# Performance work log

Hardware: AMD Instinct MI355X
Metric: run time of the kernel (lower is better)

Reference implementation:

```python
import jax, jax.numpy as jnp
import numpy as np

IN_F, D_FC, D_H = 5, 32, 64

def setup_inputs() -> dict:
    key = jax.random.key(0)
    ks = jax.random.split(key, 10)
    B, T = 4096, 512
    s_fc = 1.0 / np.sqrt(IN_F)
    s_rnn = 1.0 / np.sqrt(D_H)
    s_out = 1.0 / np.sqrt(D_H)
    return {
        "x":    jax.random.normal(ks[0], (B, T, IN_F), dtype=jnp.float32),
        "W0":   jax.random.uniform(ks[1], (D_FC, IN_F), jnp.float32, -s_fc, s_fc),
        "b0":   jax.random.uniform(ks[2], (D_FC,), jnp.float32, -s_fc, s_fc),
        "W_ih": jax.random.uniform(ks[3], (4 * D_H, D_FC), jnp.float32, -s_rnn, s_rnn),
        "W_hh": jax.random.uniform(ks[4], (4 * D_H, D_H), jnp.float32, -s_rnn, s_rnn),
        "b_ih": jax.random.uniform(ks[5], (4 * D_H,), jnp.float32, -s_rnn, s_rnn),
        "b_hh": jax.random.uniform(ks[6], (4 * D_H,), jnp.float32, -s_rnn, s_rnn),
        "Wo":   jax.random.uniform(ks[7], (1, D_H), jnp.float32, -s_out, s_out),
        "bo":   jax.random.uniform(ks[8], (1,), jnp.float32, -s_out, s_out),
    }

def reference(x, W0, b0, W_ih, W_hh, b_ih, b_hh, Wo, bo):
    B, T, _ = x.shape
    # fc0: [B,T,5] -> [B,T,32]
    h0 = x @ W0.T + b0
    # Precompute input-side gate projections for all timesteps: [B,T,4H]
    xg = h0 @ W_ih.T + (b_ih + b_hh)
    xg_t = jnp.swapaxes(xg, 0, 1)  # [T,B,4H] for scan

    def step(carry, xg_step):
        h, c = carry
        gates = xg_step + h @ W_hh.T          # [B,4H]
        i, f, g, o = jnp.split(gates, 4, axis=-1)  # PyTorch gate order i,f,g,o
        i = jax.nn.sigmoid(i)
        f = jax.nn.sigmoid(f)
        g = jnp.tanh(g)
        o = jax.nn.sigmoid(o)
        c = f * c + i * g
        h = o * jnp.tanh(c)
        return (h, c), None

    init = (jnp.zeros((B, D_H), x.dtype), jnp.zeros((B, D_H), x.dtype))
    (h_last, _), _ = jax.lax.scan(step, init, xg_t)
    # out Linear on last timestep hidden: r_out[:, -1, :] == h_last
    return h_last @ Wo.T + bo  # [B,1]
```

## Files before the change

kernel.cpp:

```cpp
#include <hip/hip_runtime.h>

#define B_TOT   4096
#define T_STEPS 512
#define IN_F    5
#define D_FC    32
#define D_H     64
#define MB      16
#define NROW    16
#define ROWE    72

typedef _Float16 h8 __attribute__((ext_vector_type(8)));
typedef __fp16   h2 __attribute__((ext_vector_type(2)));
typedef float    f4 __attribute__((ext_vector_type(4)));

__device__ __forceinline__ float fexp2(float x) { return __builtin_amdgcn_exp2f(x); }
__device__ __forceinline__ float frcp(float x)  { return __builtin_amdgcn_rcpf(x); }

__device__ __forceinline__ void lstm_cell(
    float vi, float vf, float vg, float vo,
    float nbi, float nbf, float pbg, float nbo,
    float K1, float K2,
    float& cs, _Float16* dst)
{
    const float Ei = fexp2(fmaf(-K1, vi, nbi));
    const float Eg = fexp2(fmaf( K2, vg, pbg));
    const float Eo = fexp2(fmaf(-K1, vo, nbo));
    const float fg = frcp(1.0f + fexp2(fmaf(-K1, vf, nbf)));
    const float igg = (Eg - 1.0f) * frcp((1.0f + Ei) * (1.0f + Eg));
    cs = fmaf(fg, cs, igg);
    const float Ec = fexp2(K2 * cs);
    const float h  = (Ec - 1.0f) * frcp((1.0f + Eo) * (1.0f + Ec));
    *dst = (_Float16)h;
}

__global__ __launch_bounds__(256) void lstm_mfma(
    const float* __restrict__ x,
    const float* __restrict__ W0,
    const float* __restrict__ b0,
    const float* __restrict__ W_ih,
    const float* __restrict__ W_hh,
    const float* __restrict__ b_ih,
    const float* __restrict__ b_hh,
    const float* __restrict__ Wo,
    const float* __restrict__ bo,
    float* __restrict__ out)
{
    __shared__ __align__(16) _Float16 H[2][NROW][ROWE];

    const int tid  = threadIdx.x;
    const int lane = tid & 63;
    const int w    = tid >> 6;
    const int col  = lane & 15;
    const int quad = lane >> 4;
    const int bblk = blockIdx.x * MB;

    const float K1 = 1.4426950408889634f;
    const float K2 = 2.8853900817779268f;

    h8 Bf[4][2];
    #pragma unroll
    for (int q = 0; q < 4; ++q) {
        const int row = q * 64 + w * 16 + col;
        #pragma unroll
        for (int c = 0; c < 2; ++c) {
            h8 f;
            #pragma unroll
            for (int jj = 0; jj < 8; ++jj) {
                const int k = c * 32 + quad * 8 + jj;
                f[jj] = (_Float16)W_hh[row * D_H + k];
            }
            Bf[q][c] = f;
        }
    }

    h8 Bx[4];
    #pragma unroll
    for (int q = 0; q < 4; ++q) {
        #pragma unroll
        for (int jj = 0; jj < 8; ++jj) Bx[q][jj] = (_Float16)0.0f;
    }
    if (quad == 0) {
        #pragma unroll
        for (int q = 0; q < 4; ++q) {
            const int row = q * 64 + w * 16 + col;
            #pragma unroll
            for (int jj = 0; jj < IN_F; ++jj) {
                float s = 0.0f;
                #pragma unroll
                for (int m = 0; m < D_FC; ++m)
                    s = fmaf(W_ih[row * D_FC + m], W0[m * IN_F + jj], s);
                Bx[q][jj] = (_Float16)s;
            }
        }
    }

    float sb[4];
    #pragma unroll
    for (int q = 0; q < 4; ++q) {
        const int row = q * 64 + w * 16 + col;
        float s = b_ih[row] + b_hh[row];
        #pragma unroll
        for (int m = 0; m < D_FC; ++m)
            s = fmaf(W_ih[row * D_FC + m], b0[m], s);
        sb[q] = s;
    }
    const float nbi = -K1 * sb[0];
    const float nbf = -K1 * sb[1];
    const float pbg =  K2 * sb[2];
    const float nbo = -K1 * sb[3];

    for (int i = tid; i < 2 * NROW * ROWE; i += 256)
        ((_Float16*)H)[i] = (_Float16)0.0f;

    const float* xb = x + (size_t)(bblk + col) * T_STEPS * IN_F;

    union AxU { h8 v; h2 pk[4]; };
    AxU Ax[2];
    #pragma unroll
    for (int jj = 0; jj < 8; ++jj) { Ax[0].v[jj] = (_Float16)0.0f; Ax[1].v[jj] = (_Float16)0.0f; }
    {
        const f4 v0 = *(const f4*)xb;
        const float s0 = xb[4];
        Ax[0].pk[0] = __builtin_amdgcn_cvt_pkrtz(v0[0], v0[1]);
        Ax[0].pk[1] = __builtin_amdgcn_cvt_pkrtz(v0[2], v0[3]);
        Ax[0].pk[2] = __builtin_amdgcn_cvt_pkrtz(s0, 0.0f);
    }
    f4 xv[2]; float x4[2];
    xv[0] = *(const f4*)(xb + IN_F);      x4[0] = xb[IN_F + 4];
    xv[1] = *(const f4*)(xb + 2 * IN_F);  x4[1] = xb[2 * IN_F + 4];

    f4 zk = {0.0f, 0.0f, 0.0f, 0.0f};
    float cs0 = 0.0f, cs1 = 0.0f, cs2 = 0.0f, cs3 = 0.0f;

    __syncthreads();

    for (int it = 0; it < T_STEPS / 2; ++it) {
        #pragma unroll
        for (int u = 0; u < 2; ++u) {
            const h8 A1 = *(const h8*)&H[u][col][quad * 8];
            const h8 A2 = *(const h8*)&H[u][col][32 + quad * 8];

            Ax[u ^ 1].pk[0] = __builtin_amdgcn_cvt_pkrtz(xv[u][0], xv[u][1]);
            Ax[u ^ 1].pk[1] = __builtin_amdgcn_cvt_pkrtz(xv[u][2], xv[u][3]);
            Ax[u ^ 1].pk[2] = __builtin_amdgcn_cvt_pkrtz(x4[u], 0.0f);
            {
                int tn = 2 * it + u + 3;
                tn = (tn < T_STEPS) ? tn : (T_STEPS - 1);
                const float* xp = xb + tn * IN_F;
                xv[u] = *(const f4*)xp;
                x4[u] = xp[4];
            }

            f4 acc[4];
            #pragma unroll
            for (int q = 0; q < 4; ++q)
                acc[q] = __builtin_amdgcn_mfma_f32_16x16x32_f16(Ax[u].v, Bx[q], zk, 0, 0, 0);
            #pragma unroll
            for (int q = 0; q < 4; ++q)
                acc[q] = __builtin_amdgcn_mfma_f32_16x16x32_f16(A1, Bf[q][0], acc[q], 0, 0, 0);
            #pragma unroll
            for (int q = 0; q < 4; ++q)
                acc[q] = __builtin_amdgcn_mfma_f32_16x16x32_f16(A2, Bf[q][1], acc[q], 0, 0, 0);

            lstm_cell(acc[0][0], acc[1][0], acc[2][0], acc[3][0],
                      nbi, nbf, pbg, nbo, K1, K2,
                      cs0, &H[u ^ 1][quad * 4 + 0][w * 16 + col]);
            lstm_cell(acc[0][1], acc[1][1], acc[2][1], acc[3][1],
                      nbi, nbf, pbg, nbo, K1, K2,
                      cs1, &H[u ^ 1][quad * 4 + 1][w * 16 + col]);
            lstm_cell(acc[0][2], acc[1][2], acc[2][2], acc[3][2],
                      nbi, nbf, pbg, nbo, K1, K2,
                      cs2, &H[u ^ 1][quad * 4 + 2][w * 16 + col]);
            lstm_cell(acc[0][3], acc[1][3], acc[2][3], acc[3][3],
                      nbi, nbf, pbg, nbo, K1, K2,
                      cs3, &H[u ^ 1][quad * 4 + 3][w * 16 + col]);

            asm volatile("s_waitcnt lgkmcnt(0)" ::: "memory");
            __builtin_amdgcn_s_barrier();
            asm volatile("" ::: "memory");
        }
    }

    if (tid < MB) {
        float a = bo[0];
        #pragma unroll 8
        for (int j = 0; j < D_H; ++j)
            a = fmaf((float)H[0][tid][j], Wo[j], a);
        out[bblk + tid] = a;
    }
}

extern "C" void kernel_launch(void* const* d_in, const int* in_sizes, int n_in,
                              void* d_out, int out_size, void* d_ws, size_t ws_size,
                              hipStream_t stream) {
    const float* x    = (const float*)d_in[0];
    const float* W0   = (const float*)d_in[1];
    const float* b0   = (const float*)d_in[2];
    const float* W_ih = (const float*)d_in[3];
    const float* W_hh = (const float*)d_in[4];
    const float* b_ih = (const float*)d_in[5];
    const float* b_hh = (const float*)d_in[6];
    const float* Wo   = (const float*)d_in[7];
    const float* bo   = (const float*)d_in[8];
    float* out = (float*)d_out;

    hipLaunchKernelGGL(lstm_mfma, dim3(B_TOT / MB), dim3(256), 0, stream,
                       x, W0, b0, W_ih, W_hh, b_ih, b_hh, Wo, bo, out);
}
```

Before: 318.9 us.

## Fold activation scales and bias into MFMA weights and packed-f32 gate math

Pre-scales the W_hh, fused input weights and gate biases by the exp2 constants, and feeds the bias as the initial MFMA accumulator, so the per-step fma on each gate pre-activation goes away. The cell update is rewritten to combine the forget-gate reciprocal and the input-gate product into a single reciprocal per element. Elementwise ops now use float2 vectors so the compiler can emit packed FP32 instructions. This shortens the serial per-step latency on the critical path. The cost is that the scaled weights are rounded to fp16 after scaling, and the merged denominator carries some overflow risk.

```diff
diff --git a/kernel.cpp b/kernel.cpp
--- a/kernel.cpp
+++ b/kernel.cpp
@@ -12,25 +12,58 @@
 typedef _Float16 h8 __attribute__((ext_vector_type(8)));
 typedef __fp16   h2 __attribute__((ext_vector_type(2)));
 typedef float    f4 __attribute__((ext_vector_type(4)));
+typedef float    f2 __attribute__((ext_vector_type(2)));
 
 __device__ __forceinline__ float fexp2(float x) { return __builtin_amdgcn_exp2f(x); }
 __device__ __forceinline__ float frcp(float x)  { return __builtin_amdgcn_rcpf(x); }
 
-__device__ __forceinline__ void lstm_cell(
-    float vi, float vf, float vg, float vo,
-    float nbi, float nbf, float pbg, float nbo,
-    float K1, float K2,
-    float& cs, _Float16* dst)
+__device__ __forceinline__ void lstm_cell4(
+    f2 iA, f2 fA, f2 gA, f2 oA,
+    f2 iB, f2 fB, f2 gB, f2 oB,
+    f2 pk2, f2 one,
+    f2& csA, f2& csB,
+    _Float16* d0, _Float16* d1, _Float16* d2, _Float16* d3)
 {
-    const float Ei = fexp2(fmaf(-K1, vi, nbi));
-    const float Eg = fexp2(fmaf( K2, vg, pbg));
-    const float Eo = fexp2(fmaf(-K1, vo, nbo));
-    const float fg = frcp(1.0f + fexp2(fmaf(-K1, vf, nbf)));
-    const float igg = (Eg - 1.0f) * frcp((1.0f + Ei) * (1.0f + Eg));
-    cs = fmaf(fg, cs, igg);
-    const float Ec = fexp2(K2 * cs);
-    const float h  = (Ec - 1.0f) * frcp((1.0f + Eo) * (1.0f + Ec));
-    *dst = (_Float16)h;
+    f2 EiA, EfA, EgA, EoA, EiB, EfB, EgB, EoB;
+    EiA[0]=fexp2(iA[0]); EiA[1]=fexp2(iA[1]);
+    EgA[0]=fexp2(gA[0]); EgA[1]=fexp2(gA[1]);
+    EfA[0]=fexp2(fA[0]); EfA[1]=fexp2(fA[1]);
+    EoA[0]=fexp2(oA[0]); EoA[1]=fexp2(oA[1]);
+    EiB[0]=fexp2(iB[0]); EiB[1]=fexp2(iB[1]);
+    EgB[0]=fexp2(gB[0]); EgB[1]=fexp2(gB[1]);
+    EfB[0]=fexp2(fB[0]); EfB[1]=fexp2(fB[1]);
+    EoB[0]=fexp2(oB[0]); EoB[1]=fexp2(oB[1]);
+
+    const f2 pIA = one + EiA, pFA = one + EfA, pGA = one + EgA, pOA = one + EoA;
+    const f2 pIB = one + EiB, pFB = one + EfB, pGB = one + EgB, pOB = one + EoB;
+
+    const f2 mIGA = pIA * pGA;
+    const f2 mIGB = pIB * pGB;
+    const f2 numA = csA * mIGA + (EgA - one) * pFA;
+    const f2 numB = csB * mIGB + (EgB - one) * pFB;
+    const f2 denA = mIGA * pFA;
+    const f2 denB = mIGB * pFB;
+    f2 rA, rB;
+    rA[0] = frcp(denA[0]); rA[1] = frcp(denA[1]);
+    rB[0] = frcp(denB[0]); rB[1] = frcp(denB[1]);
+    csA = numA * rA;
+    csB = numB * rB;
+    const f2 aCA = pk2 * csA;
+    const f2 aCB = pk2 * csB;
+    f2 EcA, EcB;
+    EcA[0]=fexp2(aCA[0]); EcA[1]=fexp2(aCA[1]);
+    EcB[0]=fexp2(aCB[0]); EcB[1]=fexp2(aCB[1]);
+    const f2 mOCA = pOA * (one + EcA);
+    const f2 mOCB = pOB * (one + EcB);
+    f2 r2A, r2B;
+    r2A[0] = frcp(mOCA[0]); r2A[1] = frcp(mOCA[1]);
+    r2B[0] = frcp(mOCB[0]); r2B[1] = frcp(mOCB[1]);
+    const f2 hA = (EcA - one) * r2A;
+    const f2 hB = (EcB - one) * r2B;
+    *d0 = (_Float16)hA[0];
+    *d1 = (_Float16)hA[1];
+    *d2 = (_Float16)hB[0];
+    *d3 = (_Float16)hB[1];
 }
 
 __global__ __launch_bounds__(256) void lstm_mfma(
@@ -56,6 +89,7 @@
 
     const float K1 = 1.4426950408889634f;
     const float K2 = 2.8853900817779268f;
+    const float SC[4] = { -K1, -K1, K2, -K1 };
 
     h8 Bf[4][2];
     #pragma unroll
@@ -67,7 +101,7 @@
             #pragma unroll
             for (int jj = 0; jj < 8; ++jj) {
                 const int k = c * 32 + quad * 8 + jj;
-                f[jj] = (_Float16)W_hh[row * D_H + k];
+                f[jj] = (_Float16)(W_hh[row * D_H + k] * SC[q]);
             }
             Bf[q][c] = f;
         }
@@ -89,12 +123,12 @@
                 #pragma unroll
                 for (int m = 0; m < D_FC; ++m)
                     s = fmaf(W_ih[row * D_FC + m], W0[m * IN_F + jj], s);
-                Bx[q][jj] = (_Float16)s;
+                Bx[q][jj] = (_Float16)(s * SC[q]);
             }
         }
     }
 
-    float sb[4];
+    f4 biasC[4];
     #pragma unroll
     for (int q = 0; q < 4; ++q) {
         const int row = q * 64 + w * 16 + col;
@@ -102,12 +136,12 @@
         #pragma unroll
         for (int m = 0; m < D_FC; ++m)
             s = fmaf(W_ih[row * D_FC + m], b0[m], s);
-        sb[q] = s;
-    }
-    const float nbi = -K1 * sb[0];
-    const float nbf = -K1 * sb[1];
-    const float pbg =  K2 * sb[2];
-    const float nbo = -K1 * sb[3];
+        const float sbq = s * SC[q];
+        biasC[q] = (f4){ sbq, sbq, sbq, sbq };
+    }
+
+    const f2 pk2 = {  K2,  K2 };
+    const f2 one = { 1.0f, 1.0f };
 
     for (int i = tid; i < 2 * NROW * ROWE; i += 256)
         ((_Float16*)H)[i] = (_Float16)0.0f;
@@ -129,8 +163,7 @@
     xv[0] = *(const f4*)(xb + IN_F);      x4[0] = xb[IN_F + 4];
     xv[1] = *(const f4*)(xb + 2 * IN_F);  x4[1] = xb[2 * IN_F + 4];
 
-    f4 zk = {0.0f, 0.0f, 0.0f, 0.0f};
-    float cs0 = 0.0f, cs1 = 0.0f, cs2 = 0.0f, cs3 = 0.0f;
+    f2 cs01 = {0.0f, 0.0f}, cs23 = {0.0f, 0.0f};
 
     __syncthreads();
 
@@ -154,7 +187,7 @@
             f4 acc[4];
             #pragma unroll
             for (int q = 0; q < 4; ++q)
-                acc[q] = __builtin_amdgcn_mfma_f32_16x16x32_f16(Ax[u].v, Bx[q], zk, 0, 0, 0);
+                acc[q] = __builtin_amdgcn_mfma_f32_16x16x32_f16(Ax[u].v, Bx[q], biasC[q], 0, 0, 0);
             #pragma unroll
             for (int q = 0; q < 4; ++q)
                 acc[q] = __builtin_amdgcn_mfma_f32_16x16x32_f16(A1, Bf[q][0], acc[q], 0, 0, 0);
@@ -162,18 +195,15 @@
             for (int q = 0; q < 4; ++q)
                 acc[q] = __builtin_amdgcn_mfma_f32_16x16x32_f16(A2, Bf[q][1], acc[q], 0, 0, 0);
 
-            lstm_cell(acc[0][0], acc[1][0], acc[2][0], acc[3][0],
-                      nbi, nbf, pbg, nbo, K1, K2,
-                      cs0, &H[u ^ 1][quad * 4 + 0][w * 16 + col]);
-            lstm_cell(acc[0][1], acc[1][1], acc[2][1], acc[3][1],
-                      nbi, nbf, pbg, nbo, K1, K2,
-                      cs1, &H[u ^ 1][quad * 4 + 1][w * 16 + col]);
-            lstm_cell(acc[0][2], acc[1][2], acc[2][2], acc[3][2],
-                      nbi, nbf, pbg, nbo, K1, K2,
-                      cs2, &H[u ^ 1][quad * 4 + 2][w * 16 + col]);
-            lstm_cell(acc[0][3], acc[1][3], acc[2][3], acc[3][3],
-                      nbi, nbf, pbg, nbo, K1, K2,
-                      cs3, &H[u ^ 1][quad * 4 + 3][w * 16 + col]);
+            lstm_cell4((f2){acc[0][0], acc[0][1]}, (f2){acc[1][0], acc[1][1]},
+                       (f2){acc[2][0], acc[2][1]}, (f2){acc[3][0], acc[3][1]},
+                       (f2){acc[0][2], acc[0][3]}, (f2){acc[1][2], acc[1][3]},
+                       (f2){acc[2][2], acc[2][3]}, (f2){acc[3][2], acc[3][3]},
+                       pk2, one, cs01, cs23,
+                       &H[u ^ 1][quad * 4 + 0][w * 16 + col],
+                       &H[u ^ 1][quad * 4 + 1][w * 16 + col],
+                       &H[u ^ 1][quad * 4 + 2][w * 16 + col],
+                       &H[u ^ 1][quad * 4 + 3][w * 16 + col]);
 
             asm volatile("s_waitcnt lgkmcnt(0)" ::: "memory");
             __builtin_amdgcn_s_barrier();
```

New measurement: 283.4 us. 1.13x faster.
